# Kernel optimization log

Hardware: AMD Instinct MI355X
Metric: run time of the kernel (lower is better)

## Reference

```python
import jax, jax.numpy as jnp
import numpy as np
from jax import lax

B, C, H, W = 8, 384, 64, 64


def cos_map(N):
    # ortho DCT-II basis: weight[n, x] = cos(n*(x+0.5)*pi/N) * sqrt(2/N), row 0 /= sqrt(2)
    wx = (jnp.arange(N, dtype=jnp.float32) + 0.5) / N
    wn = jnp.arange(N, dtype=jnp.float32)[:, None]
    w = jnp.cos(wn * wx[None, :] * jnp.pi) * np.sqrt(2.0 / N).astype(np.float32)
    return w.at[0, :].multiply(np.float32(1.0 / np.sqrt(2.0)))


def setup_inputs() -> dict:
    key = jax.random.key(0)
    ks = jax.random.split(key, 8)
    s = 0.05
    return {
        "x": jax.random.normal(ks[0], (B, C, H, W), jnp.float32),
        "freq_embed": jax.random.normal(ks[1], (H, W, C), jnp.float32),
        "dw_w": jax.random.normal(ks[2], (C, 1, 3, 3), jnp.float32) * s,
        "dw_b": jnp.zeros((C,), jnp.float32),
        "lin_w": jax.random.normal(ks[3], (2 * C, C), jnp.float32) * s,
        "lin_b": jnp.zeros((2 * C,), jnp.float32),
        "tok_w": jax.random.normal(ks[4], (C, C), jnp.float32) * s,
        "tok_b": jnp.zeros((C,), jnp.float32),
        "c": jnp.ones((1,), jnp.float32),
        "alpha": jnp.ones((1,), jnp.float32) * 0.1,
        "ln_g": jnp.ones((C,), jnp.float32),
        "ln_b": jnp.zeros((C,), jnp.float32),
        "out_w": jax.random.normal(ks[5], (C, C), jnp.float32) * s,
        "out_b": jnp.zeros((C,), jnp.float32),
    }


def reference(x, freq_embed, dw_w, dw_b, lin_w, lin_b, tok_w, tok_b, c, alpha, ln_g, ln_b, out_w, out_b):
    Bc, Cc, Hc, Wc = x.shape
    # depthwise 3x3 conv
    x = lax.conv_general_dilated(x, dw_w, (1, 1), 'SAME',
                                 feature_group_count=Cc,
                                 dimension_numbers=('NCHW', 'OIHW', 'NCHW'))
    x = x + dw_b[None, :, None, None]
    # linear to 2C (channels-last), split into signal x and gate z
    xz = jnp.einsum('bchw,dc->bhwd', x, lin_w) + lin_b
    xs, z = xz[..., :Cc], xz[..., Cc:]          # [B,H,W,C]
    xs = jnp.transpose(xs, (0, 3, 1, 2))        # [B,C,H,W]
    # 2D ortho DCT-II: D = Wh @ x @ Ww^T
    Wh, Ww = cos_map(Hc), cos_map(Wc)
    Xd = jnp.einsum('nh,bchw,kw->bcnk', Wh, xs, Ww)
    # learned frequency gating: t = ReLU(Linear(freq_embed)), per (H,W,C)
    t = jax.nn.relu(jnp.einsum('hwc,dc->hwd', freq_embed, tok_w) + tok_b)
    ct = jnp.transpose(jnp.cos(c * t), (2, 0, 1))[None]        # [1,C,H,W]
    st = jnp.transpose(jnp.sin(c * t), (2, 0, 1))[None] / c[0]
    # x_u0 == x_v0 == Xd in the original (dct2d applied twice to same x)
    final = ct * Xd + st * (Xd + 0.5 * alpha[0] * Xd)
    # 2D inverse DCT: x = Wh^T @ D @ Ww
    xi = jnp.einsum('nh,bcnk,kw->bchw', Wh, final, Ww)
    # LayerNorm over channels, gate with SiLU(z), output linear
    y = jnp.transpose(xi, (0, 2, 3, 1))          # [B,H,W,C]
    mu = jnp.mean(y, axis=-1, keepdims=True)
    var = jnp.mean((y - mu) ** 2, axis=-1, keepdims=True)
    y = (y - mu) * lax.rsqrt(var + 1e-5) * ln_g + ln_b
    y = y * jax.nn.silu(z)
    y = jnp.einsum('bhwc,dc->bhwd', y, out_w) + out_b
    return jnp.transpose(y, (0, 3, 1, 2))        # [B,C,H,W]
```

## Files before the change

kernel.cpp:

```cpp
#include <hip/hip_runtime.h>

typedef _Float16 h2 __attribute__((ext_vector_type(2)));
typedef _Float16 h4 __attribute__((ext_vector_type(4)));
typedef _Float16 h8 __attribute__((ext_vector_type(8)));
typedef float    f4 __attribute__((ext_vector_type(4)));

#define MFMA32(a,b,c) __builtin_amdgcn_mfma_f32_16x16x32_f16((a),(b),(c),0,0,0)
#define MFMA16(a,b,c) __builtin_amdgcn_mfma_f32_16x16x16f16((a),(b),(c),0,0,0)

#define B_N 8
#define C_N 384
#define P_N 4096
#define PI_F 3.14159265358979323846f

__device__ __forceinline__ h4 to_h4(f4 v) {
  h4 r; r[0]=(_Float16)v[0]; r[1]=(_Float16)v[1]; r[2]=(_Float16)v[2]; r[3]=(_Float16)v[3];
  return r;
}

__device__ __forceinline__ void gl_lds16(const _Float16* g, _Float16* l) {
  __builtin_amdgcn_global_load_lds(
      (const __attribute__((address_space(1))) void*)g,
      (__attribute__((address_space(3))) void*)l, 16, 0, 0);
}

__device__ __forceinline__ void gemm_step(
    const _Float16* __restrict__ ga, const _Float16* __restrict__ gb,
    int kcn, bool pref,
    _Float16* laC, _Float16* lbC, _Float16* laN, _Float16* lbN,
    f4 (&acc)[4][4]) {
  int t = threadIdx.x, lane = t & 63, wave = t >> 6;
  int quad = lane >> 4, l15 = lane & 15;
  int wm = wave >> 1, wn = wave & 1;
  int s_row = lane >> 2;
  if (pref) {
    #pragma unroll
    for (int s = 0; s < 2; s++) {
      int seg = wave * 2 + s;
      int row = seg * 16 + s_row;
      gl_lds16(ga + (size_t)row*384 + kcn, &laN[seg*512 + lane*8]);
      gl_lds16(gb + (size_t)row*384 + kcn, &lbN[seg*512 + lane*8]);
    }
    asm volatile("s_waitcnt vmcnt(4)" ::: "memory");
  } else {
    asm volatile("s_waitcnt vmcnt(0)" ::: "memory");
  }
  __builtin_amdgcn_s_barrier();
  asm volatile("" ::: "memory");
  h8 af[4], bf[4];
  int sq = (quad ^ (l15 & 3)) * 8;
  #pragma unroll
  for (int i = 0; i < 4; i++) {
    af[i] = *(const h8*)&laC[(wm*64 + i*16 + l15)*32 + sq];
    bf[i] = *(const h8*)&lbC[(wn*64 + i*16 + l15)*32 + sq];
  }
  asm volatile("s_waitcnt lgkmcnt(0)" ::: "memory");
  __builtin_amdgcn_s_barrier();
  asm volatile("" ::: "memory");
  #pragma unroll
  for (int i = 0; i < 4; i++)
  #pragma unroll
  for (int j = 0; j < 4; j++)
    acc[i][j] = MFMA32(af[i], bf[j], acc[i][j]);
}

__global__ __launch_bounds__(256) void k_setup(
    const float* __restrict__ lin_w, const float* __restrict__ tok_w,
    const float* __restrict__ out_w, _Float16* __restrict__ lwh,
    _Float16* __restrict__ twh, _Float16* __restrict__ owh,
    _Float16* __restrict__ wmg, _Float16* __restrict__ wmtg) {
  int t = blockIdx.x * 256 + threadIdx.x;
  if (t < 768*384) lwh[t] = (_Float16)lin_w[t];
  if (t < 384*384) { twh[t] = (_Float16)tok_w[t]; owh[t] = (_Float16)out_w[t]; }
  if (t < 4096) {
    int n = t >> 6, h = t & 63;
    float v = cosf((float)n * ((float)h + 0.5f) * (PI_F / 64.0f)) * 0.1767766952966369f;
    if (n == 0) v *= 0.7071067811865476f;
    wmg[n*64 + h]  = (_Float16)v;
    wmtg[h*64 + n] = (_Float16)v;
  }
}

__global__ __launch_bounds__(256) void k_dwconv(
    const float* __restrict__ x, const float* __restrict__ dww,
    const float* __restrict__ dwb, _Float16* __restrict__ xdw) {
  int blk = blockIdx.x;
  int hs = blk & 15;
  int rest = blk >> 4;
  int cgi = rest % 6;
  int b = rest / 6;
  int c0 = cgi * 64;
  int h0 = hs * 4;
  int t = threadIdx.x;
  __shared__ float wsm[576];
  __shared__ float bsm[64];
  __shared__ _Float16 buf[4][64 * 68];
  for (int i = t; i < 576; i += 256) wsm[i] = dww[c0*9 + i];
  if (t < 64) bsm[t] = dwb[c0 + t];
  __syncthreads();
  int lane = t & 63;
  int wslot = lane & 15, w4 = wslot * 4;
  int cs = t >> 4;
  bool wlo = (wslot == 0), whi = (wslot == 15);
  int lm = (lane - 1) & 63, lp = (lane + 1) & 63;
  const float* xb = x + (size_t)b * C_N * P_N + w4;
  f4 prev[4], cur[4];
  float pL[4], pR[4], cL[4], cR[4];
  #pragma unroll
  for (int q = 0; q < 4; q++) {
    const float* xc = xb + (size_t)(c0 + cs*4 + q) * P_N;
    prev[q] = (h0 > 0) ? *(const f4*)(xc + (h0-1)*64) : f4{0.f,0.f,0.f,0.f};
    cur[q]  = *(const f4*)(xc + h0*64);
    pL[q] = __shfl(prev[q][3], lm, 64); pR[q] = __shfl(prev[q][0], lp, 64);
    cL[q] = __shfl(cur[q][3],  lm, 64); cR[q] = __shfl(cur[q][0],  lp, 64);
    if (wlo) { pL[q] = 0.f; cL[q] = 0.f; }
    if (whi) { pR[q] = 0.f; cR[q] = 0.f; }
  }
  #pragma unroll
  for (int r = 0; r < 4; r++) {
    int h = h0 + r;
    float o[4][4];
    #pragma unroll
    for (int q = 0; q < 4; q++) {
      int lc = cs*4 + q;
      const float* xc = xb + (size_t)(c0 + lc) * P_N;
      f4 nxt = (h < 63) ? *(const f4*)(xc + (h+1)*64) : f4{0.f,0.f,0.f,0.f};
      float nL = __shfl(nxt[3], lm, 64), nR = __shfl(nxt[0], lp, 64);
      if (wlo) nL = 0.f;
      if (whi) nR = 0.f;
      float k0=wsm[lc*9+0],k1=wsm[lc*9+1],k2=wsm[lc*9+2];
      float k3=wsm[lc*9+3],k4=wsm[lc*9+4],k5=wsm[lc*9+5];
      float k6=wsm[lc*9+6],k7=wsm[lc*9+7],k8=wsm[lc*9+8];
      float bias = bsm[lc];
      #pragma unroll
      for (int e = 0; e < 4; e++) {
        float tl = (e > 0) ? prev[q][e-1] : pL[q];
        float tr = (e < 3) ? prev[q][e+1] : pR[q];
        float ml = (e > 0) ? cur[q][e-1]  : cL[q];
        float mr = (e < 3) ? cur[q][e+1]  : cR[q];
        float bl = (e > 0) ? nxt[e-1]     : nL;
        float br = (e < 3) ? nxt[e+1]     : nR;
        float acc = bias;
        acc += k0*tl + k1*prev[q][e] + k2*tr;
        acc += k3*ml + k4*cur[q][e]  + k5*mr;
        acc += k6*bl + k7*nxt[e]     + k8*br;
        o[q][e] = acc;
      }
      prev[q] = cur[q]; pL[q] = cL[q]; pR[q] = cR[q];
      cur[q] = nxt;     cL[q] = nL;    cR[q] = nR;
    }
    #pragma unroll
    for (int e = 0; e < 4; e++) {
      h4 hv;
      #pragma unroll
      for (int q = 0; q < 4; q++) hv[q] = (_Float16)o[q][e];
      *(h4*)&buf[r][(w4 + e) * 68 + cs * 4] = hv;
    }
  }
  __syncthreads();
  #pragma unroll
  for (int r = 0; r < 4; r++) {
    _Float16* op = xdw + ((size_t)b*P_N + (h0 + r)*64) * C_N + c0;
    #pragma unroll
    for (int i = 0; i < 4; i++) {
      int flat = (t + 256*i) * 4;
      int pix = flat >> 6, cl = flat & 63;
      *(h4*)&op[(size_t)pix*C_N + cl] = *(const h4*)&buf[r][pix*68 + cl];
    }
  }
}

__global__ __launch_bounds__(256) void k_gate(
    const float* __restrict__ fe, const _Float16* __restrict__ twh,
    const float* __restrict__ tkb, const float* __restrict__ cc,
    const float* __restrict__ aa, _Float16* __restrict__ g) {
  int pt = blockIdx.x & 63, dt = blockIdx.x >> 6;
  int p0 = pt*64, d0 = dt*64;
  int t = threadIdx.x, lane = t & 63, wave = t >> 6;
  int quad = lane >> 4, l15 = lane & 15;
  int wm_ = wave >> 1, wn = wave & 1;
  __shared__ _Float16 la[64*40], lb[64*40];
  int srow = t >> 2, scg = (t & 3) * 8;
  f4 acc[2][2] = {};
  for (int kc = 0; kc < 384; kc += 32) {
    const float* src = fe + (size_t)(p0 + srow)*384 + kc + scg;
    f4 v0 = *(const f4*)src;
    f4 v1 = *(const f4*)(src + 4);
    h8 hv;
    hv[0]=(_Float16)v0[0]; hv[1]=(_Float16)v0[1]; hv[2]=(_Float16)v0[2]; hv[3]=(_Float16)v0[3];
    hv[4]=(_Float16)v1[0]; hv[5]=(_Float16)v1[1]; hv[6]=(_Float16)v1[2]; hv[7]=(_Float16)v1[3];
    *(h8*)&la[srow*40 + scg] = hv;
    *(h8*)&lb[srow*40 + scg] = *(const h8*)&twh[(size_t)(d0 + srow)*384 + kc + scg];
    __syncthreads();
    h8 a0 = *(const h8*)&la[(wm_*32 + l15)*40 + quad*8];
    h8 a1 = *(const h8*)&la[(wm_*32 + 16 + l15)*40 + quad*8];
    h8 b0 = *(const h8*)&lb[(wn*32 + l15)*40 + quad*8];
    h8 b1 = *(const h8*)&lb[(wn*32 + 16 + l15)*40 + quad*8];
    acc[0][0] = MFMA32(a0, b0, acc[0][0]);
    acc[0][1] = MFMA32(a0, b1, acc[0][1]);
    acc[1][0] = MFMA32(a1, b0, acc[1][0]);
    acc[1][1] = MFMA32(a1, b1, acc[1][1]);
    __syncthreads();
  }
  float c0 = cc[0];
  float s1 = (1.0f + 0.5f*aa[0]) / c0;
  #pragma unroll
  for (int i = 0; i < 2; i++)
  #pragma unroll
  for (int j = 0; j < 2; j++) {
    int d  = d0 + wn*32 + j*16 + l15;
    int pl = wm_*32 + i*16 + quad*4;
    float bias = tkb[d];
    h4 hv;
    #pragma unroll
    for (int r = 0; r < 4; r++) {
      float tv = fmaxf(acc[i][j][r] + bias, 0.0f);
      hv[r] = (_Float16)(__cosf(c0*tv) + s1*__sinf(c0*tv));
    }
    *(h4*)&g[(size_t)d*P_N + p0 + pl] = hv;
  }
}

__global__ __launch_bounds__(256) void k_gemm1(
    const _Float16* __restrict__ xdw, const _Float16* __restrict__ lwh,
    const float* __restrict__ lnb, _Float16* __restrict__ xs,
    _Float16* __restrict__ zs) {
  int pt = blockIdx.x & 31;
  int rest = blockIdx.x >> 5;
  int dt = rest % 6, b = rest / 6;
  int p0 = pt * 128, d0 = dt * 128;
  int t = threadIdx.x, lane = t & 63, wave = t >> 6;
  int quad = lane >> 4, l15 = lane & 15;
  int wm = wave >> 1, wn = wave & 1;
  __shared__ _Float16 la0[128 * 32], lb0[128 * 32];
  __shared__ _Float16 la1[128 * 32], lb1[128 * 32];
  int s_row = lane >> 2;
  int scol2 = (((lane & 3) ^ (s_row & 3)) * 8);
  const _Float16* ga = xdw + ((size_t)b*P_N + p0) * 384 + scol2;
  const _Float16* gb = lwh + (size_t)d0 * 384 + scol2;
  f4 acc[4][4] = {};
  #pragma unroll
  for (int s = 0; s < 2; s++) {
    int seg = wave * 2 + s;
    int row = seg * 16 + s_row;
    gl_lds16(ga + (size_t)row*384, &la0[seg*512 + lane*8]);
    gl_lds16(gb + (size_t)row*384, &lb0[seg*512 + lane*8]);
  }
  #pragma unroll
  for (int kt = 0; kt < 6; kt++) {
    int kc = kt * 64;
    gemm_step(ga, gb, kc + 32,  true,            la0, lb0, la1, lb1, acc);
    gemm_step(ga, gb, kc + 64,  (kc + 64 < 384), la1, lb1, la0, lb0, acc);
  }
  bool isz = (d0 >= 384);
  #pragma unroll
  for (int j = 0; j < 4; j++) {
    int d = d0 + wn*64 + j*16 + l15;
    float bias = lnb[d];
    _Float16* dst = isz ? (zs + ((size_t)b*C_N + (d-384)) * P_N)
                        : (xs + ((size_t)b*C_N + d) * P_N);
    #pragma unroll
    for (int i = 0; i < 4; i++) {
      int p = p0 + wm*64 + i*16 + quad*4;
      h4 hv;
      if (isz) {
        #pragma unroll
        for (int r = 0; r < 4; r++) {
          float v = acc[i][j][r] + bias;
          v = v / (1.0f + __expf(-v));
          hv[r] = (_Float16)v;
        }
      } else {
        #pragma unroll
        for (int r = 0; r < 4; r++) hv[r] = (_Float16)(acc[i][j][r] + bias);
      }
      *(h4*)&dst[p] = hv;
    }
  }
}

__global__ __launch_bounds__(256) void k_dct(
    const _Float16* __restrict__ xs, const _Float16* __restrict__ g,
    const _Float16* __restrict__ wmg, const _Float16* __restrict__ wmtg,
    _Float16* __restrict__ xi) {
  int b = blockIdx.x / 96, cg = blockIdx.x % 96;
  int c0 = cg * 4;
  int t = threadIdx.x, wave = t >> 6, lane = t & 63;
  int quad = lane >> 4, l15 = lane & 15;
  __shared__ _Float16 wm_s[64*72];
  __shared__ _Float16 wmt_s[64*72];
  __shared__ _Float16 pb[4][64*72];
  for (int i = t; i < 512; i += 256) {
    int row = i >> 3, col = (i & 7) * 8;
    *(h8*)&wm_s[row*72 + col]  = *(const h8*)&wmg[row*64 + col];
    *(h8*)&wmt_s[row*72 + col] = *(const h8*)&wmtg[row*64 + col];
  }
  const _Float16* xsb = xs + ((size_t)b*C_N + c0) * P_N;
  for (int i = t; i < 2048; i += 256) {
    int pl = i >> 9, idx = i & 511;
    int p = idx * 8, hh = p >> 6, ww = p & 63;
    *(h8*)&pb[pl][hh*72 + ww] = *(const h8*)&xsb[(size_t)pl*P_N + p];
  }
  __syncthreads();
  h8 aS[4][2], bW[4][2];
  #pragma unroll
  for (int I = 0; I < 4; I++)
  #pragma unroll
  for (int kk = 0; kk < 2; kk++) {
    aS[I][kk] = *(const h8*)&pb[wave][(I*16 + l15)*72 + kk*32 + quad*8];
    bW[I][kk] = *(const h8*)&wm_s[(I*16 + l15)*72 + kk*32 + quad*8];
  }
  h4 t1h[4][4];
  #pragma unroll
  for (int I = 0; I < 4; I++)
  #pragma unroll
  for (int J = 0; J < 4; J++) {
    f4 a = {};
    a = MFMA32(aS[I][0], bW[J][0], a);
    a = MFMA32(aS[I][1], bW[J][1], a);
    t1h[I][J] = to_h4(a);
  }
  __syncthreads();
  const _Float16* gb = g + (size_t)c0 * P_N;
  #pragma unroll
  for (int i = 0; i < 2; i++) {
    int id = t + 256 * i;
    int pl = id >> 7;
    int r7 = id & 127;
    int n4 = (r7 >> 3) * 4;
    int k8 = (r7 & 7) * 8;
    h8 v[4];
    #pragma unroll
    for (int q = 0; q < 4; q++)
      v[q] = *(const h8*)&gb[(size_t)pl*P_N + (n4 + q)*64 + k8];
    #pragma unroll
    for (int e = 0; e < 8; e++) {
      h4 w;
      #pragma unroll
      for (int q = 0; q < 4; q++) w[q] = v[q][e];
      *(h4*)&pb[pl][(k8 + e)*72 + n4] = w;
    }
  }
  __syncthreads();
  f4 t2[4][4] = {};
  #pragma unroll
  for (int I = 0; I < 4; I++)
  #pragma unroll
  for (int K4 = 0; K4 < 4; K4++) {
    h4 af = *(const h4*)&wm_s[(I*16 + l15)*72 + K4*16 + quad*4];
    #pragma unroll
    for (int J = 0; J < 4; J++) t2[I][J] = MFMA16(af, t1h[K4][J], t2[I][J]);
  }
  h4 fh[4][4];
  #pragma unroll
  for (int I = 0; I < 4; I++)
  #pragma unroll
  for (int J = 0; J < 4; J++) {
    h4 gv4 = *(const h4*)&pb[wave][(J*16 + l15)*72 + I*16 + quad*4];
    h4 r;
    #pragma unroll
    for (int rr = 0; rr < 4; rr++)
      r[rr] = (_Float16)(t2[I][J][rr] * (float)gv4[rr]);
    fh[I][J] = r;
  }
  f4 t3[4][4] = {};
  #pragma unroll
  for (int J = 0; J < 4; J++)
  #pragma unroll
  for (int K4 = 0; K4 < 4; K4++) {
    h4 bf = *(const h4*)&wmt_s[(J*16 + l15)*72 + K4*16 + quad*4];
    #pragma unroll
    for (int I = 0; I < 4; I++) t3[I][J] = MFMA16(fh[K4][I], bf, t3[I][J]);
  }
  h4 t3h[4][4];
  #pragma unroll
  for (int I = 0; I < 4; I++)
  #pragma unroll
  for (int J = 0; J < 4; J++) t3h[I][J] = to_h4(t3[I][J]);
  f4 t4[4][4] = {};
  #pragma unroll
  for (int I = 0; I < 4; I++)
  #pragma unroll
  for (int K4 = 0; K4 < 4; K4++) {
    h4 af = *(const h4*)&wmt_s[(I*16 + l15)*72 + K4*16 + quad*4];
    #pragma unroll
    for (int J = 0; J < 4; J++) t4[I][J] = MFMA16(af, t3h[K4][J], t4[I][J]);
  }
  #pragma unroll
  for (int I = 0; I < 4; I++)
  #pragma unroll
  for (int J = 0; J < 4; J++) {
    int w0 = I*16 + quad*4, hq = J*16 + l15;
    *(h4*)&pb[wave][hq*72 + w0] = to_h4(t4[I][J]);
  }
  __syncthreads();
  _Float16* xib = xi + ((size_t)b*C_N + c0) * P_N;
  for (int i = t; i < 2048; i += 256) {
    int pl = i >> 9, idx = i & 511;
    int p = idx * 8, hh = p >> 6, ww = p & 63;
    *(h8*)&xib[(size_t)pl*P_N + p] = *(const h8*)&pb[pl][hh*72 + ww];
  }
}

__global__ __launch_bounds__(256) void k_ubuild(
    const _Float16* __restrict__ xi, const _Float16* __restrict__ zs,
    const float* __restrict__ lng, const float* __restrict__ lnbv,
    _Float16* __restrict__ u) {
  int b = blockIdx.x >> 6, pt = blockIdx.x & 63;
  int p0 = pt * 64;
  int t = threadIdx.x;
  __shared__ _Float16 ut[64 * 392];
  __shared__ float red[4][64], red2[4][64];
  __shared__ float muL[64], rsL[64];
  const _Float16* xib = xi + (size_t)b * C_N * P_N;
  #pragma unroll
  for (int i = 0; i < 3; i++) {
    int id = t + 256 * i;
    int px0 = (id & 7) * 8;
    int c4 = (id >> 3) * 4;
    h8 v[4];
    #pragma unroll
    for (int q = 0; q < 4; q++)
      v[q] = *(const h8*)&xib[(size_t)(c4 + q) * P_N + p0 + px0];
    #pragma unroll
    for (int e = 0; e < 8; e++) {
      h4 w;
      #pragma unroll
      for (int q = 0; q < 4; q++) w[q] = v[q][e];
      *(h4*)&ut[(px0 + e) * 392 + c4] = w;
    }
  }
  __syncthreads();
  int px = t & 63, seg = t >> 6;
  float s = 0.f, ss = 0.f;
  #pragma unroll
  for (int j = 0; j < 12; j++) {
    h8 v = *(const h8*)&ut[px * 392 + seg * 96 + j * 8];
    #pragma unroll
    for (int e = 0; e < 8; e++) { float f = (float)v[e]; s += f; ss += f * f; }
  }
  red[seg][px] = s; red2[seg][px] = ss;
  __syncthreads();
  if (t < 64) {
    float st  = red[0][t] + red[1][t] + red[2][t] + red[3][t];
    float sst = red2[0][t] + red2[1][t] + red2[2][t] + red2[3][t];
    float m = st * (1.f/384.f);
    float var = sst * (1.f/384.f) - m * m;
    muL[t] = m; rsL[t] = rsqrtf(var + 1e-5f);
  }
  __syncthreads();
  const _Float16* zb = zs + (size_t)b * C_N * P_N;
  #pragma unroll
  for (int i = 0; i < 3; i++) {
    int id = t + 256 * i;
    int px0 = (id & 7) * 8;
    int c4 = (id >> 3) * 4;
    f4 g4 = *(const f4*)&lng[c4];
    f4 b4 = *(const f4*)&lnbv[c4];
    h8 z[4];
    #pragma unroll
    for (int q = 0; q < 4; q++)
      z[q] = *(const h8*)&zb[(size_t)(c4 + q) * P_N + p0 + px0];
    #pragma unroll
    for (int e = 0; e < 8; e++) {
      int p = px0 + e;
      h4 y = *(const h4*)&ut[p * 392 + c4];
      float mu = muL[p], rs = rsL[p];
      #pragma unroll
      for (int q = 0; q < 4; q++) {
        float f = ((float)y[q] - mu) * rs * g4[q] + b4[q];
        y[q] = (_Float16)(f * (float)z[q][e]);
      }
      *(h4*)&ut[p * 392 + c4] = y;
    }
  }
  __syncthreads();
  _Float16* ub = u + ((size_t)b * P_N + p0) * C_N;
  #pragma unroll
  for (int i = 0; i < 12; i++) {
    int idx = t + 256 * i;
    int row = idx / 48, ch = idx % 48;
    *(h8*)&ub[(size_t)row * C_N + ch * 8] = *(const h8*)&ut[row * 392 + ch * 8];
  }
}

__global__ __launch_bounds__(256) void k_gemm2(
    const _Float16* __restrict__ u, const _Float16* __restrict__ owh,
    const float* __restrict__ ob, float* __restrict__ out) {
  int pt = blockIdx.x & 31;
  int rest = blockIdx.x >> 5;
  int dt = rest % 3, b = rest / 3;
  int p0 = pt * 128, d0 = dt * 128;
  int t = threadIdx.x, lane = t & 63, wave = t >> 6;
  int quad = lane >> 4, l15 = lane & 15;
  int wm = wave >> 1, wn = wave & 1;
  __shared__ _Float16 la0[128 * 32], lb0[128 * 32];
  __shared__ _Float16 la1[128 * 32], lb1[128 * 32];
  int s_row = lane >> 2;
  int scol2 = (((lane & 3) ^ (s_row & 3)) * 8);
  const _Float16* ga = u   + ((size_t)b*P_N + p0) * 384 + scol2;
  const _Float16* gb = owh + (size_t)d0 * 384 + scol2;
  f4 acc[4][4] = {};
  #pragma unroll
  for (int s = 0; s < 2; s++) {
    int seg = wave * 2 + s;
    int row = seg * 16 + s_row;
    gl_lds16(ga + (size_t)row*384, &la0[seg*512 + lane*8]);
    gl_lds16(gb + (size_t)row*384, &lb0[seg*512 + lane*8]);
  }
  #pragma unroll
  for (int kt = 0; kt < 6; kt++) {
    int kc = kt * 64;
    gemm_step(ga, gb, kc + 32,  true,            la0, lb0, la1, lb1, acc);
    gemm_step(ga, gb, kc + 64,  (kc + 64 < 384), la1, lb1, la0, lb0, acc);
  }
  #pragma unroll
  for (int j = 0; j < 4; j++) {
    int d = d0 + wn*64 + j*16 + l15;
    float bias = ob[d];
    #pragma unroll
    for (int i = 0; i < 4; i++) {
      int p = p0 + wm*64 + i*16 + quad*4;
      f4 v;
      #pragma unroll
      for (int r = 0; r < 4; r++) v[r] = acc[i][j][r] + bias;
      *(f4*)&out[((size_t)b*C_N + d)*P_N + p] = v;
    }
  }
}

extern "C" void kernel_launch(void* const* d_in, const int* in_sizes, int n_in,
                              void* d_out, int out_size, void* d_ws, size_t ws_size,
                              hipStream_t stream) {
  (void)in_sizes; (void)n_in; (void)out_size; (void)ws_size;
  const float* x    = (const float*)d_in[0];
  const float* fe   = (const float*)d_in[1];
  const float* dww  = (const float*)d_in[2];
  const float* dwb  = (const float*)d_in[3];
  const float* linw = (const float*)d_in[4];
  const float* linb = (const float*)d_in[5];
  const float* tokw = (const float*)d_in[6];
  const float* tokb = (const float*)d_in[7];
  const float* cc   = (const float*)d_in[8];
  const float* aa   = (const float*)d_in[9];
  const float* lng  = (const float*)d_in[10];
  const float* lnbv = (const float*)d_in[11];
  const float* outw = (const float*)d_in[12];
  const float* outb = (const float*)d_in[13];
  float* out = (float*)d_out;

  char* ws = (char*)d_ws;
  size_t off = 0;
  auto alloc = [&](size_t bytes) -> void* {
    void* p = ws + off;
    off += (bytes + 255) & ~(size_t)255;
    return p;
  };
  _Float16* lwh  = (_Float16*)alloc((size_t)768*384*2);
  _Float16* twh  = (_Float16*)alloc((size_t)384*384*2);
  _Float16* owh  = (_Float16*)alloc((size_t)384*384*2);
  _Float16* wmg  = (_Float16*)alloc((size_t)64*64*2);
  _Float16* wmtg = (_Float16*)alloc((size_t)64*64*2);
  _Float16* xdw  = (_Float16*)alloc((size_t)B_N*P_N*C_N*2);
  _Float16* xs   = (_Float16*)alloc((size_t)B_N*C_N*P_N*2);
  _Float16* zs   = (_Float16*)alloc((size_t)B_N*C_N*P_N*2);
  _Float16* gg   = (_Float16*)alloc((size_t)C_N*P_N*2);
  _Float16* xi   = xdw;
  _Float16* uu   = xs;

  k_setup<<<1152, 256, 0, stream>>>(linw, tokw, outw, lwh, twh, owh, wmg, wmtg);
  k_dwconv<<<768, 256, 0, stream>>>(x, dww, dwb, xdw);
  k_gate<<<384, 256, 0, stream>>>(fe, twh, tokb, cc, aa, gg);
  k_gemm1<<<1536, 256, 0, stream>>>(xdw, lwh, linb, xs, zs);
  k_dct<<<768, 256, 0, stream>>>(xs, gg, wmg, wmtg, xi);
  k_ubuild<<<512, 256, 0, stream>>>(xi, zs, lng, lnbv, uu);
  k_gemm2<<<768, 256, 0, stream>>>(uu, owh, outb, out);
}
```

Baseline: 232.9 us.

## Fuse LayerNorm/gate u-build with output GEMM, keeping u tile in LDS

Merges k_ubuild and k_gemm2 into a single kernel. The 64-pixel by 384-channel LDS tile produced by the LayerNorm and SiLU gate stage now feeds MFMAs directly, with each wave computing 96 output channels. Weight fragments are read straight from global memory. This removes the fp16 write and re-read of the u intermediate and one kernel launch. In exchange it loses the double-buffered, LDS-staged pipelined GEMM, uses larger per-wave accumulators (4x6) that raise register pressure, and runs only 512 blocks.

```diff
diff --git a/kernel.cpp b/kernel.cpp
--- a/kernel.cpp
+++ b/kernel.cpp
@@ -402,10 +402,11 @@
   }
 }
 
-__global__ __launch_bounds__(256) void k_ubuild(
+__global__ __launch_bounds__(256) void k_fuse(
     const _Float16* __restrict__ xi, const _Float16* __restrict__ zs,
     const float* __restrict__ lng, const float* __restrict__ lnbv,
-    _Float16* __restrict__ u) {
+    const _Float16* __restrict__ owh, const float* __restrict__ ob,
+    float* __restrict__ out) {
   int b = blockIdx.x >> 6, pt = blockIdx.x & 63;
   int p0 = pt * 64;
   int t = threadIdx.x;
@@ -475,56 +476,37 @@
     }
   }
   __syncthreads();
-  _Float16* ub = u + ((size_t)b * P_N + p0) * C_N;
-  #pragma unroll
-  for (int i = 0; i < 12; i++) {
-    int idx = t + 256 * i;
-    int row = idx / 48, ch = idx % 48;
-    *(h8*)&ub[(size_t)row * C_N + ch * 8] = *(const h8*)&ut[row * 392 + ch * 8];
-  }
-}
-
-__global__ __launch_bounds__(256) void k_gemm2(
-    const _Float16* __restrict__ u, const _Float16* __restrict__ owh,
-    const float* __restrict__ ob, float* __restrict__ out) {
-  int pt = blockIdx.x & 31;
-  int rest = blockIdx.x >> 5;
-  int dt = rest % 3, b = rest / 3;
-  int p0 = pt * 128, d0 = dt * 128;
-  int t = threadIdx.x, lane = t & 63, wave = t >> 6;
+  int lane = t & 63, wave = t >> 6;
   int quad = lane >> 4, l15 = lane & 15;
-  int wm = wave >> 1, wn = wave & 1;
-  __shared__ _Float16 la0[128 * 32], lb0[128 * 32];
-  __shared__ _Float16 la1[128 * 32], lb1[128 * 32];
-  int s_row = lane >> 2;
-  int scol2 = (((lane & 3) ^ (s_row & 3)) * 8);
-  const _Float16* ga = u   + ((size_t)b*P_N + p0) * 384 + scol2;
-  const _Float16* gb = owh + (size_t)d0 * 384 + scol2;
-  f4 acc[4][4] = {};
-  #pragma unroll
-  for (int s = 0; s < 2; s++) {
-    int seg = wave * 2 + s;
-    int row = seg * 16 + s_row;
-    gl_lds16(ga + (size_t)row*384, &la0[seg*512 + lane*8]);
-    gl_lds16(gb + (size_t)row*384, &lb0[seg*512 + lane*8]);
-  }
-  #pragma unroll
-  for (int kt = 0; kt < 6; kt++) {
-    int kc = kt * 64;
-    gemm_step(ga, gb, kc + 32,  true,            la0, lb0, la1, lb1, acc);
-    gemm_step(ga, gb, kc + 64,  (kc + 64 < 384), la1, lb1, la0, lb0, acc);
-  }
-  #pragma unroll
-  for (int j = 0; j < 4; j++) {
-    int d = d0 + wn*64 + j*16 + l15;
+  int n0 = wave * 96;
+  f4 acc[4][6] = {};
+  const _Float16* bw = owh + (size_t)(n0 + l15) * 384 + quad * 8;
+  #pragma unroll
+  for (int kc = 0; kc < 384; kc += 32) {
+    h8 af[4], bf[6];
+    #pragma unroll
+    for (int i = 0; i < 4; i++)
+      af[i] = *(const h8*)&ut[(i*16 + l15) * 392 + kc + quad*8];
+    #pragma unroll
+    for (int j = 0; j < 6; j++)
+      bf[j] = *(const h8*)&bw[(size_t)(j*16) * 384 + kc];
+    #pragma unroll
+    for (int i = 0; i < 4; i++)
+    #pragma unroll
+    for (int j = 0; j < 6; j++)
+      acc[i][j] = MFMA32(af[i], bf[j], acc[i][j]);
+  }
+  #pragma unroll
+  for (int j = 0; j < 6; j++) {
+    int d = n0 + j*16 + l15;
     float bias = ob[d];
+    float* op = out + ((size_t)b*C_N + d) * P_N + p0;
     #pragma unroll
     for (int i = 0; i < 4; i++) {
-      int p = p0 + wm*64 + i*16 + quad*4;
       f4 v;
       #pragma unroll
       for (int r = 0; r < 4; r++) v[r] = acc[i][j][r] + bias;
-      *(f4*)&out[((size_t)b*C_N + d)*P_N + p] = v;
+      *(f4*)&op[i*16 + quad*4] = v;
     }
   }
 }
@@ -566,13 +548,11 @@
   _Float16* zs   = (_Float16*)alloc((size_t)B_N*C_N*P_N*2);
   _Float16* gg   = (_Float16*)alloc((size_t)C_N*P_N*2);
   _Float16* xi   = xdw;
-  _Float16* uu   = xs;
 
   k_setup<<<1152, 256, 0, stream>>>(linw, tokw, outw, lwh, twh, owh, wmg, wmtg);
   k_dwconv<<<768, 256, 0, stream>>>(x, dww, dwb, xdw);
   k_gate<<<384, 256, 0, stream>>>(fe, twh, tokb, cc, aa, gg);
   k_gemm1<<<1536, 256, 0, stream>>>(xdw, lwh, linb, xs, zs);
   k_dct<<<768, 256, 0, stream>>>(xs, gg, wmg, wmtg, xi);
-  k_ubuild<<<512, 256, 0, stream>>>(xi, zs, lng, lnbv, uu);
-  k_gemm2<<<768, 256, 0, stream>>>(uu, owh, outb, out);
-}
+  k_fuse<<<512, 256, 0, stream>>>(xi, zs, lng, lnbv, owh, outb, out);
+}
```

Result: no change. 229.6 us (-1.4%).
